# Kernel optimization log

Hardware: AMD Instinct MI355X
Metric: run time of the kernel (lower is better)

The kernel has to match this reference:

```python
import jax, jax.numpy as jnp
import numpy as np

B, N, D, C, H = 32, 36, 2048, 4, 512  # batch, regions, feat dim, coord dim, fusion hidden


def setup_inputs() -> dict:
    key = jax.random.key(0)
    ks = jax.random.split(key, 8)
    w = lambda k, sh: jax.random.normal(k, sh, dtype=jnp.float32) * 0.02
    return {
        "mm": jax.random.normal(ks[0], (B, N, D), dtype=jnp.float32),
        "coords": jax.random.uniform(ks[1], (B, N, C), dtype=jnp.float32),
        # MLB fusion params for coords: z = (x@W_cl * y@W_cr) @ W_cout
        "W_cl": w(ks[2], (C, H)),
        "W_cr": w(ks[3], (C, H)),
        "W_cout": w(ks[4], (H, D)),
        # MLB fusion params for features
        "W_fl": w(ks[5], (D, H)),
        "W_fr": w(ks[6], (D, H)),
        "W_fout": w(ks[7], (H, D)),
    }


def reference(mm, coords, W_cl, W_cr, W_cout, W_fl, W_fr, W_fout):
    # Project once per region (avoids projecting inside the N*N expand).
    cl = coords @ W_cl            # [B,N,H]
    cr = coords @ W_cr            # [B,N,H]
    fl = mm @ W_fl                # [B,N,H]
    fr = mm @ W_fr                # [B,N,H]
    # All-pairs bilinear fusion: Rij = f_coord(c_i, c_j) + f_feat(m_i, m_j)
    pair_c = cl[:, :, None, :] * cr[:, None, :, :]   # [B,N,N,H]
    pair_f = fl[:, :, None, :] * fr[:, None, :, :]   # [B,N,N,H]
    Rij = (jnp.einsum('bijh,hd->bijd', pair_c, W_cout)
           + jnp.einsum('bijh,hd->bijd', pair_f, W_fout))  # [B,N,N,D]
    # agg['type'] == 'max': reduce over the right (j) region axis
    mm_new = Rij.max(axis=2)      # [B,N,D]
    # residual
    return mm_new + mm
```

## Files before the change

### kernel.cpp

```cpp
#include <hip/hip_runtime.h>


typedef __attribute__((ext_vector_type(8))) short short8;
typedef __attribute__((ext_vector_type(4))) short short4v;
typedef __attribute__((ext_vector_type(4))) float f32x4;

__device__ __forceinline__ float bf2f(unsigned short h) {
  return __uint_as_float(((unsigned int)h) << 16);
}
__device__ __forceinline__ unsigned short f2bf(float f) {
  unsigned int u = __float_as_uint(f);
  u += 0x7FFFu + ((u >> 16) & 1u);
  return (unsigned short)(u >> 16);
}
__device__ __forceinline__ void gl2lds16(const void* g, void* l) {
  __builtin_amdgcn_global_load_lds(
      (const __attribute__((address_space(1))) unsigned int*)g,
      (__attribute__((address_space(3))) unsigned int*)l, 16, 0, 0);
}

__global__ __launch_bounds__(256) void k_prep(
    const float* __restrict__ mm, const float* __restrict__ Wfout,
    const float* __restrict__ Wcl, const float* __restrict__ Wcr,
    const float* __restrict__ Wcout, const float* __restrict__ Wfl,
    const float* __restrict__ Wfr, unsigned short* __restrict__ mmb,
    unsigned short* __restrict__ WS, unsigned short* __restrict__ WS2) {
  const int bid = blockIdx.x;
  if (bid < 2304) {
    int idx = bid * 256 + threadIdx.x;
    int row = idx >> 9, h = idx & 511;
    float4 m4 = *(const float4*)(mm + (size_t)row * 2048 + h * 4);
    short4v o;
    o[0] = (short)f2bf(m4.x); o[1] = (short)f2bf(m4.y);
    o[2] = (short)f2bf(m4.z); o[3] = (short)f2bf(m4.w);
    *(short4v*)(mmb + (size_t)row * 2048 + h * 4) = o;
  } else {
    int gi = (bid - 2304) * 256 + threadIdx.x;
    if (gi < 139264) {
      int n = gi & 15, qv = (gi >> 4) & 3, rest = gi >> 6;
      int kc = rest % 17, g2 = rest / 17;
      int d = g2 * 16 + n;
      short8 o;
      if (kc < 16) {
        int kbase = kc * 32 + qv * 8;
        const float* src = Wfout + (size_t)kbase * 2048 + d;
#pragma unroll
        for (int e = 0; e < 8; ++e) o[e] = (short)f2bf(src[(size_t)e * 2048]);
      } else if (qv < 2) {
        float acc[8];
#pragma unroll
        for (int e = 0; e < 8; ++e) acc[e] = 0.f;
        for (int h = 0; h < 512; ++h) {
          float wo = Wcout[(size_t)h * 2048 + d];
          float c0 = Wcl[(qv * 2 + 0) * 512 + h] * wo;
          float c1 = Wcl[(qv * 2 + 1) * 512 + h] * wo;
          float r0 = Wcr[h], r1 = Wcr[512 + h];
          float r2 = Wcr[1024 + h], r3 = Wcr[1536 + h];
          acc[0] += c0 * r0; acc[1] += c0 * r1;
          acc[2] += c0 * r2; acc[3] += c0 * r3;
          acc[4] += c1 * r0; acc[5] += c1 * r1;
          acc[6] += c1 * r2; acc[7] += c1 * r3;
        }
#pragma unroll
        for (int e = 0; e < 8; ++e) o[e] = (short)f2bf(acc[e]);
      } else {
#pragma unroll
        for (int e = 0; e < 8; ++e) o[e] = 0;
      }
      *(short8*)(WS + (size_t)gi * 8) = o;
    } else {
      int gj = gi - 139264;
      int n = gj & 15, qv = (gj >> 4) & 3, kc = (gj >> 6) & 63, cg = gj >> 12;
      int col = cg * 16 + n;
      int dbase = kc * 32 + qv * 8;
      const float* src = (col < 512) ? (Wfl + (size_t)dbase * 512 + col)
                                     : (Wfr + (size_t)dbase * 512 + (col - 512));
      short8 o;
#pragma unroll
      for (int e = 0; e < 8; ++e) o[e] = (short)f2bf(src[(size_t)e * 512]);
      *(short8*)(WS2 + (size_t)gj * 8) = o;
    }
  }
}

__global__ __launch_bounds__(256) void k_proj_feat(
    const unsigned short* __restrict__ mmb, const unsigned short* __restrict__ WS2,
    unsigned short* __restrict__ Fl, unsigned short* __restrict__ Fr) {
  const int tid = threadIdx.x;
  const int lane = tid & 63, w = tid >> 6;
  const int n = lane & 15, q = lane >> 4;
  const int m0 = blockIdx.y * 16;
  const int cg = blockIdx.x * 4 + w;
  const int c0 = cg * 16;

  f32x4 acc = {0.f, 0.f, 0.f, 0.f};
#pragma unroll 4
  for (int kc = 0; kc < 64; ++kc) {
    short8 a = *(const short8*)(mmb + (size_t)(m0 + n) * 2048 + kc * 32 + q * 8);
    short8 b = *(const short8*)(WS2 + (size_t)(cg * 64 + kc) * 512 + lane * 8);
    acc = __builtin_amdgcn_mfma_f32_16x16x32_bf16(a, b, acc, 0, 0, 0);
  }
#pragma unroll
  for (int e = 0; e < 4; ++e) {
    int row = m0 + q * 4 + e;
    int col = c0 + n;
    unsigned short v = f2bf(acc[e]);
    if (col < 512) Fl[(size_t)row * 512 + col] = v;
    else           Fr[(size_t)row * 512 + (col - 512)] = v;
  }
}

__global__ __launch_bounds__(256) void k_prod(
    const unsigned short* __restrict__ Fl, const unsigned short* __restrict__ Fr,
    const float* __restrict__ coords, unsigned short* __restrict__ Pf) {
  int idx = blockIdx.x * 256 + threadIdx.x;
  int lane = idx & 63;
  int gran = idx >> 6;
  int qg = gran / 153;
  int rem = gran - qg * 153;
  int kc = rem / 9;
  int t = rem - kc * 9;
  int n = lane & 15, q = lane >> 4;
  int b = qg / 9;
  int g, j;
  if (t < 8) { g = qg * 4 + (t >> 1); j = (t & 1) * 16 + n; }
  else       { g = qg * 4 + (n >> 2); j = 32 + (n & 3); }
  int rowj = b * 36 + j;
  short8 p;
  if (kc < 16) {
    int k0 = kc * 32 + q * 8;
    short8 cl8 = *(const short8*)(Fl + (size_t)g * 512 + k0);
    short8 cr8 = *(const short8*)(Fr + (size_t)rowj * 512 + k0);
#pragma unroll
    for (int e = 0; e < 8; ++e)
      p[e] = (short)f2bf(bf2f((unsigned short)cl8[e]) * bf2f((unsigned short)cr8[e]));
  } else if (q < 2) {
    float4 ci = *(const float4*)(coords + (size_t)g * 4);
    float4 cj = *(const float4*)(coords + (size_t)rowj * 4);
#pragma unroll
    for (int e = 0; e < 8; ++e) {
      int a = q * 2 + (e >> 2);
      float ca = (a == 0) ? ci.x : (a == 1) ? ci.y : (a == 2) ? ci.z : ci.w;
      float cb = ((e & 3) == 0) ? cj.x : ((e & 3) == 1) ? cj.y
               : ((e & 3) == 2) ? cj.z : cj.w;
      p[e] = (short)f2bf(ca * cb);
    }
  } else {
#pragma unroll
    for (int e = 0; e < 8; ++e) p[e] = 0;
  }
  *(short8*)(Pf + (size_t)idx * 8) = p;
}

__global__ __launch_bounds__(512, 4) void k_pairwise(
    const unsigned short* __restrict__ Pf, const unsigned short* __restrict__ WS,
    const float* __restrict__ mm, float* __restrict__ out) {
  __shared__ __align__(16) unsigned short lB[2][9 * 512];

  const int tid = threadIdx.x;
  const int lane = tid & 63, w = tid >> 6;
  const int n = lane & 15, q = lane >> 4;
  const int bx = blockIdx.x;
  const int x = bx & 7;
  const int m = bx >> 3;
  const int dt = m & 7;
  const int qg = x * 36 + (m >> 3);
  const int g0 = qg * 4;

  f32x4 acc[9][2];
#pragma unroll
  for (int t = 0; t < 9; ++t)
#pragma unroll
    for (int r = 0; r < 2; ++r) acc[t][r] = (f32x4){0.f, 0.f, 0.f, 0.f};

  const unsigned short* Abase = WS + ((size_t)(dt * 16 + w * 2) * 17) * 512 + lane * 8;
  const unsigned short* Bbase = Pf + (size_t)qg * 17 * 9 * 512;

  short8 aR[2], aN[2];
  gl2lds16(Bbase + (size_t)w * 512 + lane * 8, &lB[0][w * 512]);
  if (w == 0) gl2lds16(Bbase + (size_t)8 * 512 + lane * 8, &lB[0][8 * 512]);
  aR[0] = *(const short8*)(Abase);
  aR[1] = *(const short8*)(Abase + 17 * 512);
  __syncthreads();

#pragma unroll 2
  for (int kc = 0; kc < 16; ++kc) {
    const int buf = kc & 1;
    const unsigned short* bn = Bbase + (size_t)((kc + 1) * 9) * 512 + lane * 8;
    gl2lds16(bn + (size_t)w * 512, &lB[buf ^ 1][w * 512]);
    if (w == 0) gl2lds16(bn + (size_t)8 * 512, &lB[buf ^ 1][8 * 512]);
    aN[0] = *(const short8*)(Abase + (size_t)(kc + 1) * 512);
    aN[1] = *(const short8*)(Abase + (size_t)(17 + kc + 1) * 512);

    short8 bb[9];
#pragma unroll
    for (int t = 0; t < 9; ++t)
      bb[t] = *(const short8*)(&lB[buf][t * 512 + lane * 8]);
#pragma unroll
    for (int t = 0; t < 9; ++t) {
      acc[t][0] = __builtin_amdgcn_mfma_f32_16x16x32_bf16(aR[0], bb[t], acc[t][0], 0, 0, 0);
      acc[t][1] = __builtin_amdgcn_mfma_f32_16x16x32_bf16(aR[1], bb[t], acc[t][1], 0, 0, 0);
    }
    __syncthreads();
    aR[0] = aN[0];
    aR[1] = aN[1];
  }

  {
    short8 bb[9];
#pragma unroll
    for (int t = 0; t < 9; ++t)
      bb[t] = *(const short8*)(&lB[0][t * 512 + lane * 8]);
#pragma unroll
    for (int t = 0; t < 9; ++t) {
      acc[t][0] = __builtin_amdgcn_mfma_f32_16x16x32_bf16(aR[0], bb[t], acc[t][0], 0, 0, 0);
      acc[t][1] = __builtin_amdgcn_mfma_f32_16x16x32_bf16(aR[1], bb[t], acc[t][1], 0, 0, 0);
    }
  }

#pragma unroll
  for (int r = 0; r < 2; ++r) {
#pragma unroll
    for (int e = 0; e < 4; ++e) {
      float vs = acc[8][r][e];
#pragma unroll
      for (int ii = 0; ii < 4; ++ii) {
        float v = fmaxf(acc[ii * 2][r][e], acc[ii * 2 + 1][r][e]);
        v = fmaxf(v, ((n >> 2) == ii) ? vs : -1e30f);
#pragma unroll
        for (int s = 1; s < 16; s <<= 1) v = fmaxf(v, __shfl_xor(v, s, 64));
        if (n == 0) {
          int d = dt * 256 + w * 32 + r * 16 + q * 4 + e;
          size_t o = (size_t)(g0 + ii) * 2048 + d;
          out[o] = v + mm[o];
        }
      }
    }
  }
}

extern "C" void kernel_launch(void* const* d_in, const int* in_sizes, int n_in,
                              void* d_out, int out_size, void* d_ws, size_t ws_size,
                              hipStream_t stream) {
  const float* mm     = (const float*)d_in[0];
  const float* coords = (const float*)d_in[1];
  const float* Wcl    = (const float*)d_in[2];
  const float* Wcr    = (const float*)d_in[3];
  const float* Wcout  = (const float*)d_in[4];
  const float* Wfl    = (const float*)d_in[5];
  const float* Wfr    = (const float*)d_in[6];
  const float* Wfout  = (const float*)d_in[7];
  float* out = (float*)d_out;

  unsigned short* Fl  = (unsigned short*)d_ws;
  unsigned short* Fr  = Fl + (size_t)1152 * 512;
  unsigned short* WS  = Fr + (size_t)1152 * 512;
  unsigned short* WS2 = WS + (size_t)139264 * 8;
  unsigned short* mmb = WS2 + (size_t)262144 * 8;
  unsigned short* Pf  = mmb + (size_t)1152 * 2048;

  k_prep<<<2304 + 1568, 256, 0, stream>>>(mm, Wfout, Wcl, Wcr, Wcout,
                                          Wfl, Wfr, mmb, WS, WS2);
  k_proj_feat<<<dim3(16, 72), 256, 0, stream>>>(mmb, WS2, Fl, Fr);
  k_prod<<<11016, 256, 0, stream>>>(Fl, Fr, coords, Pf);
  k_pairwise<<<2304, 512, 0, stream>>>(Pf, WS, mm, out);
}
```

Measured before the change: 293.4 us.

## Triple-buffer LDS B tiles with prefetch depth two and partial vmcnt waits

Moves the pairwise MFMA kernel from double to triple buffering of the B tiles in LDS, prefetching two k-chunks ahead. The full __syncthreads is replaced by a partial s_waitcnt vmcnt plus s_barrier, so global-to-LDS loads can stay in flight across iterations. This costs more LDS per block, which may limit occupancy. It also depends on hand-counted vmcnt values, which are fragile if the compiler reorders memory operations.

After: 337.1 us. 14.9% more time.

```diff
diff --git a/kernel.cpp b/kernel.cpp
--- a/kernel.cpp
+++ b/kernel.cpp
@@ -155,7 +155,7 @@
 __global__ __launch_bounds__(512, 4) void k_pairwise(
     const unsigned short* __restrict__ Pf, const unsigned short* __restrict__ WS,
     const float* __restrict__ mm, float* __restrict__ out) {
-  __shared__ __align__(16) unsigned short lB[2][9 * 512];
+  __shared__ __align__(16) unsigned short lB[3][9 * 512];
 
   const int tid = threadIdx.x;
   const int lane = tid & 63, w = tid >> 6;
@@ -179,38 +179,63 @@
   short8 aR[2], aN[2];
   gl2lds16(Bbase + (size_t)w * 512 + lane * 8, &lB[0][w * 512]);
   if (w == 0) gl2lds16(Bbase + (size_t)8 * 512 + lane * 8, &lB[0][8 * 512]);
+  {
+    const unsigned short* b1 = Bbase + (size_t)9 * 512 + lane * 8;
+    gl2lds16(b1 + (size_t)w * 512, &lB[1][w * 512]);
+    if (w == 0) gl2lds16(b1 + (size_t)8 * 512, &lB[1][8 * 512]);
+  }
   aR[0] = *(const short8*)(Abase);
   aR[1] = *(const short8*)(Abase + 17 * 512);
   __syncthreads();
 
-#pragma unroll 2
-  for (int kc = 0; kc < 16; ++kc) {
-    const int buf = kc & 1;
-    const unsigned short* bn = Bbase + (size_t)((kc + 1) * 9) * 512 + lane * 8;
-    gl2lds16(bn + (size_t)w * 512, &lB[buf ^ 1][w * 512]);
-    if (w == 0) gl2lds16(bn + (size_t)8 * 512, &lB[buf ^ 1][8 * 512]);
+#pragma unroll 3
+  for (int kc = 0; kc < 15; ++kc) {
+    const unsigned short* bn = Bbase + (size_t)((kc + 2) * 9) * 512 + lane * 8;
+    gl2lds16(bn + (size_t)w * 512, &lB[(kc + 2) % 3][w * 512]);
+    if (w == 0) gl2lds16(bn + (size_t)8 * 512, &lB[(kc + 2) % 3][8 * 512]);
     aN[0] = *(const short8*)(Abase + (size_t)(kc + 1) * 512);
     aN[1] = *(const short8*)(Abase + (size_t)(17 + kc + 1) * 512);
 
     short8 bb[9];
 #pragma unroll
     for (int t = 0; t < 9; ++t)
-      bb[t] = *(const short8*)(&lB[buf][t * 512 + lane * 8]);
+      bb[t] = *(const short8*)(&lB[kc % 3][t * 512 + lane * 8]);
 #pragma unroll
     for (int t = 0; t < 9; ++t) {
       acc[t][0] = __builtin_amdgcn_mfma_f32_16x16x32_bf16(aR[0], bb[t], acc[t][0], 0, 0, 0);
       acc[t][1] = __builtin_amdgcn_mfma_f32_16x16x32_bf16(aR[1], bb[t], acc[t][1], 0, 0, 0);
     }
-    __syncthreads();
+    asm volatile("s_waitcnt vmcnt(3)" ::: "memory");
+    __builtin_amdgcn_s_barrier();
+    __builtin_amdgcn_sched_barrier(0);
     aR[0] = aN[0];
     aR[1] = aN[1];
   }
 
   {
+    aN[0] = *(const short8*)(Abase + (size_t)16 * 512);
+    aN[1] = *(const short8*)(Abase + (size_t)(17 + 16) * 512);
     short8 bb[9];
 #pragma unroll
     for (int t = 0; t < 9; ++t)
       bb[t] = *(const short8*)(&lB[0][t * 512 + lane * 8]);
+#pragma unroll
+    for (int t = 0; t < 9; ++t) {
+      acc[t][0] = __builtin_amdgcn_mfma_f32_16x16x32_bf16(aR[0], bb[t], acc[t][0], 0, 0, 0);
+      acc[t][1] = __builtin_amdgcn_mfma_f32_16x16x32_bf16(aR[1], bb[t], acc[t][1], 0, 0, 0);
+    }
+    asm volatile("s_waitcnt vmcnt(2)" ::: "memory");
+    __builtin_amdgcn_s_barrier();
+    __builtin_amdgcn_sched_barrier(0);
+    aR[0] = aN[0];
+    aR[1] = aN[1];
+  }
+
+  {
+    short8 bb[9];
+#pragma unroll
+    for (int t = 0; t < 9; ++t)
+      bb[t] = *(const short8*)(&lB[1][t * 512 + lane * 8]);
 #pragma unroll
     for (int t = 0; t < 9; ++t) {
       acc[t][0] = __builtin_amdgcn_mfma_f32_16x16x32_bf16(aR[0], bb[t], acc[t][0], 0, 0, 0);
```

## Fuse pairwise product generation into the pairwise GEMM kernel, dropping Pf buffer

Applied to the files above, without the earlier changes.

Removes the separate k_prod kernel that materialized the Fl*Fr and coordinate outer products to global memory. The pairwise kernel now computes these bf16 products on the fly from Fl/Fr/coords into an LDS ring buffer. Cross-region slices and the coordinate term are precomputed once per block into dedicated LDS areas, and the coord K-chunk is handled as a final extra MFMA step. This cuts a large global write/read and one launch, but adds VALU conversion work and more LDS inside the MFMA loop, plus an unroll pragma in the prep reduction.

Measured after the change: 338.0 us. +15.2%, slower.

```diff
diff --git a/kernel.cpp b/kernel.cpp
--- a/kernel.cpp
+++ b/kernel.cpp
@@ -13,10 +13,13 @@
   u += 0x7FFFu + ((u >> 16) & 1u);
   return (unsigned short)(u >> 16);
 }
-__device__ __forceinline__ void gl2lds16(const void* g, void* l) {
-  __builtin_amdgcn_global_load_lds(
-      (const __attribute__((address_space(1))) unsigned int*)g,
-      (__attribute__((address_space(3))) unsigned int*)l, 16, 0, 0);
+
+__device__ __forceinline__ short8 prod8(short8 cl, short8 cr) {
+  short8 p;
+#pragma unroll
+  for (int e = 0; e < 8; ++e)
+    p[e] = (short)f2bf(bf2f((unsigned short)cl[e]) * bf2f((unsigned short)cr[e]));
+  return p;
 }
 
 __global__ __launch_bounds__(256) void k_prep(
@@ -50,6 +53,7 @@
         float acc[8];
 #pragma unroll
         for (int e = 0; e < 8; ++e) acc[e] = 0.f;
+#pragma unroll 4
         for (int h = 0; h < 512; ++h) {
           float wo = Wcout[(size_t)h * 2048 + d];
           float c0 = Wcl[(qv * 2 + 0) * 512 + h] * wo;
@@ -110,52 +114,13 @@
   }
 }
 
-__global__ __launch_bounds__(256) void k_prod(
+__global__ __launch_bounds__(512, 4) void k_pairwise(
     const unsigned short* __restrict__ Fl, const unsigned short* __restrict__ Fr,
-    const float* __restrict__ coords, unsigned short* __restrict__ Pf) {
-  int idx = blockIdx.x * 256 + threadIdx.x;
-  int lane = idx & 63;
-  int gran = idx >> 6;
-  int qg = gran / 153;
-  int rem = gran - qg * 153;
-  int kc = rem / 9;
-  int t = rem - kc * 9;
-  int n = lane & 15, q = lane >> 4;
-  int b = qg / 9;
-  int g, j;
-  if (t < 8) { g = qg * 4 + (t >> 1); j = (t & 1) * 16 + n; }
-  else       { g = qg * 4 + (n >> 2); j = 32 + (n & 3); }
-  int rowj = b * 36 + j;
-  short8 p;
-  if (kc < 16) {
-    int k0 = kc * 32 + q * 8;
-    short8 cl8 = *(const short8*)(Fl + (size_t)g * 512 + k0);
-    short8 cr8 = *(const short8*)(Fr + (size_t)rowj * 512 + k0);
-#pragma unroll
-    for (int e = 0; e < 8; ++e)
-      p[e] = (short)f2bf(bf2f((unsigned short)cl8[e]) * bf2f((unsigned short)cr8[e]));
-  } else if (q < 2) {
-    float4 ci = *(const float4*)(coords + (size_t)g * 4);
-    float4 cj = *(const float4*)(coords + (size_t)rowj * 4);
-#pragma unroll
-    for (int e = 0; e < 8; ++e) {
-      int a = q * 2 + (e >> 2);
-      float ca = (a == 0) ? ci.x : (a == 1) ? ci.y : (a == 2) ? ci.z : ci.w;
-      float cb = ((e & 3) == 0) ? cj.x : ((e & 3) == 1) ? cj.y
-               : ((e & 3) == 2) ? cj.z : cj.w;
-      p[e] = (short)f2bf(ca * cb);
-    }
-  } else {
-#pragma unroll
-    for (int e = 0; e < 8; ++e) p[e] = 0;
-  }
-  *(short8*)(Pf + (size_t)idx * 8) = p;
-}
-
-__global__ __launch_bounds__(512, 4) void k_pairwise(
-    const unsigned short* __restrict__ Pf, const unsigned short* __restrict__ WS,
+    const float* __restrict__ coords, const unsigned short* __restrict__ WS,
     const float* __restrict__ mm, float* __restrict__ out) {
-  __shared__ __align__(16) unsigned short lB[2][9 * 512];
+  __shared__ __align__(16) unsigned short ring[2][8 * 512];
+  __shared__ __align__(16) unsigned short g8[16 * 512];
+  __shared__ __align__(16) unsigned short c16[9 * 512];
 
   const int tid = threadIdx.x;
   const int lane = tid & 63, w = tid >> 6;
@@ -166,6 +131,7 @@
   const int dt = m & 7;
   const int qg = x * 36 + (m >> 3);
   const int g0 = qg * 4;
+  const int b36 = (qg / 9) * 36;
 
   f32x4 acc[9][2];
 #pragma unroll
@@ -174,47 +140,117 @@
     for (int r = 0; r < 2; ++r) acc[t][r] = (f32x4){0.f, 0.f, 0.f, 0.f};
 
   const unsigned short* Abase = WS + ((size_t)(dt * 16 + w * 2) * 17) * 512 + lane * 8;
-  const unsigned short* Bbase = Pf + (size_t)qg * 17 * 9 * 512;
+
+  const int gp = g0 + (w >> 1);
+  const int jp = (w & 1) * 16 + n;
+  const unsigned short* FlP = Fl + (size_t)gp * 512 + q * 8;
+  const unsigned short* FrP = Fr + (size_t)(b36 + jp) * 512 + q * 8;
+  const int gs = g0 + (n >> 2);
+  const int js = 32 + (n & 3);
 
   short8 aR[2], aN[2];
-  gl2lds16(Bbase + (size_t)w * 512 + lane * 8, &lB[0][w * 512]);
-  if (w == 0) gl2lds16(Bbase + (size_t)8 * 512 + lane * 8, &lB[0][8 * 512]);
+
+  {
+    short8 cl = *(const short8*)(FlP);
+    short8 cr = *(const short8*)(FrP);
+    *(short8*)(&ring[0][w * 512 + lane * 8]) = prod8(cl, cr);
+  }
+#pragma unroll
+  for (int si = 0; si < 2; ++si) {
+    int s = w + si * 8;
+    short8 cl = *(const short8*)(Fl + (size_t)gs * 512 + s * 32 + q * 8);
+    short8 cr = *(const short8*)(Fr + (size_t)(b36 + js) * 512 + s * 32 + q * 8);
+    *(short8*)(&g8[s * 512 + lane * 8]) = prod8(cl, cr);
+  }
+  {
+    short8 cp;
+    if (q < 2) {
+      float4 ci = *(const float4*)(coords + (size_t)gp * 4);
+      float4 cj = *(const float4*)(coords + (size_t)(b36 + jp) * 4);
+#pragma unroll
+      for (int e = 0; e < 8; ++e) {
+        int a = q * 2 + (e >> 2);
+        float ca = (a == 0) ? ci.x : (a == 1) ? ci.y : (a == 2) ? ci.z : ci.w;
+        float cb = ((e & 3) == 0) ? cj.x : ((e & 3) == 1) ? cj.y
+                 : ((e & 3) == 2) ? cj.z : cj.w;
+        cp[e] = (short)f2bf(ca * cb);
+      }
+    } else {
+#pragma unroll
+      for (int e = 0; e < 8; ++e) cp[e] = 0;
+    }
+    *(short8*)(&c16[w * 512 + lane * 8]) = cp;
+    if (w == 0) {
+      short8 cs;
+      if (q < 2) {
+        float4 ci = *(const float4*)(coords + (size_t)gs * 4);
+        float4 cj = *(const float4*)(coords + (size_t)(b36 + js) * 4);
+#pragma unroll
+        for (int e = 0; e < 8; ++e) {
+          int a = q * 2 + (e >> 2);
+          float ca = (a == 0) ? ci.x : (a == 1) ? ci.y : (a == 2) ? ci.z : ci.w;
+          float cb = ((e & 3) == 0) ? cj.x : ((e & 3) == 1) ? cj.y
+                   : ((e & 3) == 2) ? cj.z : cj.w;
+          cs[e] = (short)f2bf(ca * cb);
+        }
+      } else {
+#pragma unroll
+        for (int e = 0; e < 8; ++e) cs[e] = 0;
+      }
+      *(short8*)(&c16[8 * 512 + lane * 8]) = cs;
+    }
+  }
   aR[0] = *(const short8*)(Abase);
   aR[1] = *(const short8*)(Abase + 17 * 512);
   __syncthreads();
 
 #pragma unroll 2
-  for (int kc = 0; kc < 16; ++kc) {
-    const int buf = kc & 1;
-    const unsigned short* bn = Bbase + (size_t)((kc + 1) * 9) * 512 + lane * 8;
-    gl2lds16(bn + (size_t)w * 512, &lB[buf ^ 1][w * 512]);
-    if (w == 0) gl2lds16(bn + (size_t)8 * 512, &lB[buf ^ 1][8 * 512]);
-    aN[0] = *(const short8*)(Abase + (size_t)(kc + 1) * 512);
-    aN[1] = *(const short8*)(Abase + (size_t)(17 + kc + 1) * 512);
+  for (int c = 0; c < 15; ++c) {
+    const int buf = c & 1;
+    short8 cl = *(const short8*)(FlP + (c + 1) * 32);
+    short8 cr = *(const short8*)(FrP + (c + 1) * 32);
+    aN[0] = *(const short8*)(Abase + (size_t)(c + 1) * 512);
+    aN[1] = *(const short8*)(Abase + (size_t)(17 + c + 1) * 512);
 
     short8 bb[9];
 #pragma unroll
-    for (int t = 0; t < 9; ++t)
-      bb[t] = *(const short8*)(&lB[buf][t * 512 + lane * 8]);
+    for (int t = 0; t < 8; ++t)
+      bb[t] = *(const short8*)(&ring[buf][t * 512 + lane * 8]);
+    bb[8] = *(const short8*)(&g8[c * 512 + lane * 8]);
 #pragma unroll
     for (int t = 0; t < 9; ++t) {
       acc[t][0] = __builtin_amdgcn_mfma_f32_16x16x32_bf16(aR[0], bb[t], acc[t][0], 0, 0, 0);
       acc[t][1] = __builtin_amdgcn_mfma_f32_16x16x32_bf16(aR[1], bb[t], acc[t][1], 0, 0, 0);
     }
+    *(short8*)(&ring[buf ^ 1][w * 512 + lane * 8]) = prod8(cl, cr);
     __syncthreads();
     aR[0] = aN[0];
     aR[1] = aN[1];
   }
 
   {
+    aN[0] = *(const short8*)(Abase + (size_t)16 * 512);
+    aN[1] = *(const short8*)(Abase + (size_t)(17 + 16) * 512);
     short8 bb[9];
 #pragma unroll
-    for (int t = 0; t < 9; ++t)
-      bb[t] = *(const short8*)(&lB[0][t * 512 + lane * 8]);
+    for (int t = 0; t < 8; ++t)
+      bb[t] = *(const short8*)(&ring[1][t * 512 + lane * 8]);
+    bb[8] = *(const short8*)(&g8[15 * 512 + lane * 8]);
 #pragma unroll
     for (int t = 0; t < 9; ++t) {
       acc[t][0] = __builtin_amdgcn_mfma_f32_16x16x32_bf16(aR[0], bb[t], acc[t][0], 0, 0, 0);
       acc[t][1] = __builtin_amdgcn_mfma_f32_16x16x32_bf16(aR[1], bb[t], acc[t][1], 0, 0, 0);
+    }
+  }
+  {
+    short8 bb[9];
+#pragma unroll
+    for (int t = 0; t < 9; ++t)
+      bb[t] = *(const short8*)(&c16[t * 512 + lane * 8]);
+#pragma unroll
+    for (int t = 0; t < 9; ++t) {
+      acc[t][0] = __builtin_amdgcn_mfma_f32_16x16x32_bf16(aN[0], bb[t], acc[t][0], 0, 0, 0);
+      acc[t][1] = __builtin_amdgcn_mfma_f32_16x16x32_bf16(aN[1], bb[t], acc[t][1], 0, 0, 0);
     }
   }
 
@@ -257,11 +293,9 @@
   unsigned short* WS  = Fr + (size_t)1152 * 512;
   unsigned short* WS2 = WS + (size_t)139264 * 8;
   unsigned short* mmb = WS2 + (size_t)262144 * 8;
-  unsigned short* Pf  = mmb + (size_t)1152 * 2048;
 
   k_prep<<<2304 + 1568, 256, 0, stream>>>(mm, Wfout, Wcl, Wcr, Wcout,
                                           Wfl, Wfr, mmb, WS, WS2);
   k_proj_feat<<<dim3(16, 72), 256, 0, stream>>>(mmb, WS2, Fl, Fr);
-  k_prod<<<11016, 256, 0, stream>>>(Fl, Fr, coords, Pf);
-  k_pairwise<<<2304, 512, 0, stream>>>(Pf, WS, mm, out);
-}
+  k_pairwise<<<2304, 512, 0, stream>>>(Fl, Fr, coords, WS, mm, out);
+}
```
